# Optimization experiments

Hardware: AMD Instinct MI355X
Metric: run time of the kernel (lower is better)

Reference implementation:

```python
import jax, jax.numpy as jnp
import numpy as np

DIM, EXP = 512, 16
INTERNAL = DIM * EXP  # 8192
BATCH, SEQ = 2, 2048


def setup_inputs() -> dict:
    key = jax.random.key(0)
    ks = jax.random.split(key, 8)
    s = 0.02
    return {
        "x": jax.random.normal(ks[0], (BATCH, SEQ, DIM), jnp.float32),
        "W_dt_w": jax.random.normal(ks[1], (INTERNAL, DIM), jnp.float32) * s,
        "W_dt_b": jnp.zeros((INTERNAL,), jnp.float32),
        "W_B_w": jax.random.normal(ks[2], (INTERNAL, DIM), jnp.float32) * s,
        "W_B_b": jnp.zeros((INTERNAL,), jnp.float32),
        "W_C_w": jax.random.normal(ks[3], (INTERNAL, DIM), jnp.float32) * s,
        "W_C_b": jnp.zeros((INTERNAL,), jnp.float32),
        "W_V_w": jax.random.normal(ks[4], (INTERNAL, DIM), jnp.float32) * s,
        "W_V_b": jnp.zeros((INTERNAL,), jnp.float32),
        # A_log = -rand(internal): negative for stability, as in torch init
        "A_log": -jax.random.uniform(ks[5], (INTERNAL,), jnp.float32),
        "W_out_w": jax.random.normal(ks[6], (DIM, INTERNAL), jnp.float32) * s,
        "W_out_b": jnp.zeros((DIM,), jnp.float32),
    }


def _scan_combine(c1, c2):
    # semi-separable recurrence h_t = a_t * h_{t-1} + b_t, as associative op
    a1, b1 = c1
    a2, b2 = c2
    return a2 * a1, a2 * b1 + b2


def reference(x, W_dt_w, W_dt_b, W_B_w, W_B_b, W_C_w, W_C_b,
              W_V_w, W_V_b, A_log, W_out_w, W_out_b):
    # Featurizer10: discretized SSM features. Shapes: x [b,s,d] -> [b,s,n]
    dt = jax.nn.softplus(jnp.einsum('bsd,nd->bsn', x, W_dt_w) + W_dt_b)
    A_bar = jnp.exp(dt * A_log)                                  # S: [b,s,n]
    B_bar = dt * (jnp.einsum('bsd,nd->bsn', x, W_B_w) + W_B_b)   # B: [b,s,n]
    C = jnp.einsum('bsd,nd->bsn', x, W_C_w) + W_C_b              # C: [b,s,n]
    V = jnp.einsum('bsd,nd->bsn', x, W_V_w) + W_V_b              # V: [b,s,n]
    # Token mixing: h_t = A_bar_t * h_{t-1} + B_bar_t * V_t (parallel scan)
    u = B_bar * V
    _, h = jax.lax.associative_scan(_scan_combine, (A_bar, u), axis=1)
    y = C * h                                                    # [b,s,n]
    # Output projection back to model dim
    return jnp.einsum('bsn,dn->bsd', y, W_out_w) + W_out_b
```

## Files before the change

kernel.cpp:

```cpp
#include <hip/hip_runtime.h>

#define DIMK 512
#define NCH  8192
#define MTOT 4096
#define SEQL 2048
#define KS   4

typedef __attribute__((ext_vector_type(8))) short bf16x8;
typedef __attribute__((ext_vector_type(4))) float f32x4;
typedef unsigned int uint32;

__device__ __forceinline__ unsigned short f2bf(float f) {
  unsigned int u = __float_as_uint(f);
  u += 0x7fffu + ((u >> 16) & 1u);
  return (unsigned short)(u >> 16);
}
__device__ __forceinline__ float bf2f(unsigned short v) {
  return __uint_as_float(((unsigned int)v) << 16);
}

struct CvtArgs {
  const float* src[6];
  unsigned short* dst[6];
  int cum[7];
};
__global__ __launch_bounds__(256) void cvt_all_kernel(CvtArgs a, int tot) {
  const int stride = gridDim.x * 256;
  for (int i = blockIdx.x * 256 + threadIdx.x; i < tot; i += stride) {
    int s = 0;
    while (i >= a.cum[s + 1]) ++s;
    const int j = i - a.cum[s];
    const float4* sp = reinterpret_cast<const float4*>(a.src[s]);
    float4 v0 = sp[2 * j], v1 = sp[2 * j + 1];
    union { unsigned short us[8]; uint4 v; } o;
    o.us[0] = f2bf(v0.x); o.us[1] = f2bf(v0.y); o.us[2] = f2bf(v0.z); o.us[3] = f2bf(v0.w);
    o.us[4] = f2bf(v1.x); o.us[5] = f2bf(v1.y); o.us[6] = f2bf(v1.z); o.us[7] = f2bf(v1.w);
    reinterpret_cast<uint4*>(a.dst[s])[j] = o.v;
  }
}

__device__ __forceinline__ int swz(int row, int q) { return q ^ ((row >> 2) & 3); }

#define PLDS_A 4096
#define PLDS_W 8192
#define PLDS   (PLDS_A + PLDS_W)
__global__ __launch_bounds__(256) void proj_kernel(
    const unsigned short* __restrict__ xb,
    const unsigned short* __restrict__ w4,
    const float* __restrict__ b_dt, const float* __restrict__ b_B,
    const float* __restrict__ b_C, const float* __restrict__ b_V,
    const float* __restrict__ A_log,
    uint32* __restrict__ au,
    unsigned short* __restrict__ c_out)
{
  __shared__ __align__(16) unsigned short lds[2][PLDS];
  const int tid = threadIdx.x;
  const int lane = tid & 63;
  const int wave = tid >> 6;
  const int wr = wave >> 1, wc = wave & 1;
  const int n0 = blockIdx.x * 64;
  const int m0 = blockIdx.y * 128;

  auto stage = [&](int buf, int kt) {
    const int k0 = kt * 32;
    #pragma unroll
    for (int i = 0; i < 2; ++i) {
      int c = i * 256 + tid;
      int row = c >> 2, q = c & 3;
      const unsigned short* g = xb + (size_t)(m0 + row) * DIMK + k0 + swz(row, q) * 8;
      __builtin_amdgcn_global_load_lds(
          (const __attribute__((address_space(1))) void*)g,
          (__attribute__((address_space(3))) void*)&lds[buf][c * 8], 16, 0, 0);
    }
    #pragma unroll
    for (int p = 0; p < 4; ++p) {
      int row = tid >> 2, q = tid & 3;
      const unsigned short* g = w4 + ((size_t)p * NCH + n0 + row) * DIMK + k0 + swz(row, q) * 8;
      __builtin_amdgcn_global_load_lds(
          (const __attribute__((address_space(1))) void*)g,
          (__attribute__((address_space(3))) void*)&lds[buf][PLDS_A + p * 2048 + tid * 8], 16, 0, 0);
    }
  };

  f32x4 acc[4][4][2];
  #pragma unroll
  for (int p = 0; p < 4; ++p)
    #pragma unroll
    for (int fm = 0; fm < 4; ++fm)
      #pragma unroll
      for (int fn = 0; fn < 2; ++fn)
        acc[p][fm][fn] = (f32x4){0.f, 0.f, 0.f, 0.f};

  stage(0, 0);
  constexpr int NKT = DIMK / 32;
  #pragma unroll 1
  for (int kt = 0; kt < NKT; ++kt) {
    const int buf = kt & 1;
    if (kt + 1 < NKT) {
      stage(buf ^ 1, kt + 1);
      asm volatile("s_waitcnt vmcnt(6)" ::: "memory");
    } else {
      asm volatile("s_waitcnt vmcnt(0)" ::: "memory");
    }
    __builtin_amdgcn_s_barrier();

    const int arow = wr * 64 + (lane & 15);
    const int qq = lane >> 4;
    bf16x8 af[4];
    #pragma unroll
    for (int fm = 0; fm < 4; ++fm) {
      const int r = arow + fm * 16;
      af[fm] = *reinterpret_cast<const bf16x8*>(&lds[buf][r * 32 + swz(r, qq) * 8]);
    }
    #pragma unroll
    for (int p = 0; p < 4; ++p) {
      bf16x8 bfr[2];
      #pragma unroll
      for (int fn = 0; fn < 2; ++fn) {
        const int r = wc * 32 + fn * 16 + (lane & 15);
        bfr[fn] = *reinterpret_cast<const bf16x8*>(
            &lds[buf][PLDS_A + p * 2048 + r * 32 + swz(r, qq) * 8]);
      }
      __builtin_amdgcn_s_setprio(1);
      #pragma unroll
      for (int fm = 0; fm < 4; ++fm)
        #pragma unroll
        for (int fn = 0; fn < 2; ++fn)
          acc[p][fm][fn] = __builtin_amdgcn_mfma_f32_16x16x32_bf16(
              af[fm], bfr[fn], acc[p][fm][fn], 0, 0, 0);
      __builtin_amdgcn_s_setprio(0);
    }
    asm volatile("s_waitcnt lgkmcnt(0)" ::: "memory");
    __builtin_amdgcn_s_barrier();
  }

  #pragma unroll
  for (int fn = 0; fn < 2; ++fn) {
    const int n = n0 + wc * 32 + fn * 16 + (lane & 15);
    const float vbdt = b_dt[n], vbB = b_B[n], vbC = b_C[n], vbV = b_V[n];
    const float al = A_log[n];
    #pragma unroll
    for (int fm = 0; fm < 4; ++fm) {
      const int mbase = m0 + wr * 64 + fm * 16 + (lane >> 4) * 4;
      #pragma unroll
      for (int r = 0; r < 4; ++r) {
        const size_t off = (size_t)(mbase + r) * NCH + n;
        const float zdt = acc[0][fm][fn][r] + vbdt;
        const float zB  = acc[1][fm][fn][r] + vbB;
        const float zC  = acc[2][fm][fn][r] + vbC;
        const float zV  = acc[3][fm][fn][r] + vbV;
        const float dt = (zdt > 15.f) ? zdt : __logf(1.f + __expf(zdt));
        au[off] = ((uint32)f2bf(dt * al) << 16) | (uint32)f2bf(dt * zB * zV);
        c_out[off] = f2bf(zC);
      }
    }
  }
}

#define SCH 16
#define CSTEPS 128
__global__ __launch_bounds__(1024) void scan_kernel(
    const uint32* __restrict__ au,
    unsigned short* cy)
{
  __shared__ float Ap[SCH][64], He[SCH][64], H0[SCH][64];
  const int lane = threadIdx.x & 63;
  const int w = threadIdx.x >> 6;
  const int c = blockIdx.x * 64 + lane;
  const size_t base = (size_t)blockIdx.y * SEQL * NCH + (size_t)(w * CSTEPS) * NCH + c;

  {
    const uint32* ap = au + base;
    float h = 0.f, vsum = 0.f;
    #pragma unroll 1
    for (int s = 0; s < CSTEPS; s += 8) {
      uint32 wv[8];
      #pragma unroll
      for (int i = 0; i < 8; ++i) wv[i] = ap[(size_t)(s + i) * NCH];
      #pragma unroll
      for (int i = 0; i < 8; ++i) {
        const float av = bf2f((unsigned short)(wv[i] >> 16));
        const float uv = bf2f((unsigned short)(wv[i] & 0xffff));
        vsum += av;
        h = fmaf(__expf(av), h, uv);
      }
    }
    Ap[w][lane] = __expf(vsum);
    He[w][lane] = h;
  }
  __syncthreads();
  if (w == 0) {
    float run = 0.f;
    #pragma unroll
    for (int jj = 0; jj < SCH; ++jj) {
      H0[jj][lane] = run;
      run = fmaf(Ap[jj][lane], run, He[jj][lane]);
    }
  }
  __syncthreads();
  {
    const uint32* ap = au + base;
    unsigned short* cp = cy + base;
    float h = H0[w][lane];
    #pragma unroll 1
    for (int s = 0; s < CSTEPS; s += 8) {
      uint32 wv[8];
      float cv[8];
      #pragma unroll
      for (int i = 0; i < 8; ++i) {
        wv[i] = ap[(size_t)(s + i) * NCH];
        cv[i] = bf2f(cp[(size_t)(s + i) * NCH]);
      }
      #pragma unroll
      for (int i = 0; i < 8; ++i) {
        const float av = bf2f((unsigned short)(wv[i] >> 16));
        const float uv = bf2f((unsigned short)(wv[i] & 0xffff));
        h = fmaf(__expf(av), h, uv);
        cv[i] *= h;
      }
      #pragma unroll
      for (int i = 0; i < 8; ++i) cp[(size_t)(s + i) * NCH] = f2bf(cv[i]);
    }
  }
}

#define OLDS_A 4096
#define OLDS_B 2048
#define OLDS   (OLDS_A + OLDS_B)
__global__ __launch_bounds__(256) void outproj_kernel(
    const unsigned short* __restrict__ yb,
    const unsigned short* __restrict__ wout,
    float* __restrict__ partial)
{
  __shared__ __align__(16) unsigned short lds[2][OLDS];
  const int tid = threadIdx.x;
  const int lane = tid & 63;
  const int wave = tid >> 6;
  const int wr = wave >> 1, wc = wave & 1;
  const int m0 = blockIdx.x * 128;
  const int d0 = blockIdx.y * 64;
  const int kbase = blockIdx.z * (NCH / KS);

  auto stage = [&](int buf, int kt) {
    const int k0 = kbase + kt * 32;
    #pragma unroll
    for (int i = 0; i < 2; ++i) {
      int c = i * 256 + tid;
      int row = c >> 2, q = c & 3;
      const unsigned short* g = yb + (size_t)(m0 + row) * NCH + k0 + swz(row, q) * 8;
      __builtin_amdgcn_global_load_lds(
          (const __attribute__((address_space(1))) void*)g,
          (__attribute__((address_space(3))) void*)&lds[buf][c * 8], 16, 0, 0);
    }
    {
      int row = tid >> 2, q = tid & 3;
      const unsigned short* g = wout + (size_t)(d0 + row) * NCH + k0 + swz(row, q) * 8;
      __builtin_amdgcn_global_load_lds(
          (const __attribute__((address_space(1))) void*)g,
          (__attribute__((address_space(3))) void*)&lds[buf][OLDS_A + tid * 8], 16, 0, 0);
    }
  };

  f32x4 acc[4][2];
  #pragma unroll
  for (int fm = 0; fm < 4; ++fm)
    #pragma unroll
    for (int fn = 0; fn < 2; ++fn) acc[fm][fn] = (f32x4){0.f, 0.f, 0.f, 0.f};

  stage(0, 0);
  constexpr int NKT = (NCH / KS) / 32;
  #pragma unroll 1
  for (int kt = 0; kt < NKT; ++kt) {
    const int buf = kt & 1;
    if (kt + 1 < NKT) {
      stage(buf ^ 1, kt + 1);
      asm volatile("s_waitcnt vmcnt(3)" ::: "memory");
    } else {
      asm volatile("s_waitcnt vmcnt(0)" ::: "memory");
    }
    __builtin_amdgcn_s_barrier();

    const int qq = lane >> 4;
    bf16x8 af[4], bfr[2];
    #pragma unroll
    for (int fm = 0; fm < 4; ++fm) {
      const int r = wr * 64 + fm * 16 + (lane & 15);
      af[fm] = *reinterpret_cast<const bf16x8*>(&lds[buf][r * 32 + swz(r, qq) * 8]);
    }
    #pragma unroll
    for (int fn = 0; fn < 2; ++fn) {
      const int r = wc * 32 + fn * 16 + (lane & 15);
      bfr[fn] = *reinterpret_cast<const bf16x8*>(
          &lds[buf][OLDS_A + r * 32 + swz(r, qq) * 8]);
    }
    __builtin_amdgcn_s_setprio(1);
    #pragma unroll
    for (int fm = 0; fm < 4; ++fm)
      #pragma unroll
      for (int fn = 0; fn < 2; ++fn)
        acc[fm][fn] = __builtin_amdgcn_mfma_f32_16x16x32_bf16(
            af[fm], bfr[fn], acc[fm][fn], 0, 0, 0);
    __builtin_amdgcn_s_setprio(0);
    asm volatile("s_waitcnt lgkmcnt(0)" ::: "memory");
    __builtin_amdgcn_s_barrier();
  }

  float* pout = partial + (size_t)blockIdx.z * MTOT * DIMK;
  #pragma unroll
  for (int fn = 0; fn < 2; ++fn) {
    const int d = d0 + wc * 32 + fn * 16 + (lane & 15);
    #pragma unroll
    for (int fm = 0; fm < 4; ++fm) {
      const int mbase = m0 + wr * 64 + fm * 16 + (lane >> 4) * 4;
      #pragma unroll
      for (int r = 0; r < 4; ++r)
        pout[(size_t)(mbase + r) * DIMK + d] = acc[fm][fn][r];
    }
  }
}

__global__ __launch_bounds__(256) void reduce_kernel(
    const float* __restrict__ p, const float* __restrict__ bias,
    float* __restrict__ out)
{
  const int i = blockIdx.x * 256 + threadIdx.x;
  const float4* p4 = reinterpret_cast<const float4*>(p);
  float4 s = p4[i];
  #pragma unroll
  for (int k = 1; k < KS; ++k) {
    float4 t = p4[(size_t)k * (MTOT * DIMK / 4) + i];
    s.x += t.x; s.y += t.y; s.z += t.z; s.w += t.w;
  }
  const float4 b = reinterpret_cast<const float4*>(bias)[i & 127];
  s.x += b.x; s.y += b.y; s.z += b.z; s.w += b.w;
  reinterpret_cast<float4*>(out)[i] = s;
}

extern "C" void kernel_launch(void* const* d_in, const int* in_sizes, int n_in,
                              void* d_out, int out_size, void* d_ws, size_t ws_size,
                              hipStream_t stream) {
  const float* x    = (const float*)d_in[0];
  const float* Wdt  = (const float*)d_in[1];
  const float* bdt  = (const float*)d_in[2];
  const float* WB   = (const float*)d_in[3];
  const float* bB   = (const float*)d_in[4];
  const float* WC   = (const float*)d_in[5];
  const float* bC   = (const float*)d_in[6];
  const float* WV   = (const float*)d_in[7];
  const float* bV   = (const float*)d_in[8];
  const float* Alog = (const float*)d_in[9];
  const float* Wout = (const float*)d_in[10];
  const float* bout = (const float*)d_in[11];
  float* out = (float*)d_out;

  char* ws = (char*)d_ws;
  unsigned short* woutb = (unsigned short*)(ws);
  unsigned short* xb    = (unsigned short*)(ws + 8388608);
  unsigned short* w4    = (unsigned short*)(ws + 12582912);
  char* dyn = ws + 46137344;
  uint32*         au  = (uint32*)(dyn);
  unsigned short* cy  = (unsigned short*)(dyn + (size_t)MTOT * NCH * 4);
  float* partial = (float*)au;

  CvtArgs ca;
  ca.src[0] = x;    ca.dst[0] = xb;
  ca.src[1] = Wdt;  ca.dst[1] = w4 + 0 * 4194304;
  ca.src[2] = WB;   ca.dst[2] = w4 + 1 * 4194304;
  ca.src[3] = WC;   ca.dst[3] = w4 + 2 * 4194304;
  ca.src[4] = WV;   ca.dst[4] = w4 + 3 * 4194304;
  ca.src[5] = Wout; ca.dst[5] = woutb;
  ca.cum[0] = 0;        ca.cum[1] = 262144;  ca.cum[2] = 786432;
  ca.cum[3] = 1310720;  ca.cum[4] = 1835008; ca.cum[5] = 2359296;
  ca.cum[6] = 2883584;
  cvt_all_kernel<<<2048, 256, 0, stream>>>(ca, 2883584);

  proj_kernel<<<dim3(NCH / 64, MTOT / 128), 256, 0, stream>>>(
      xb, w4, bdt, bB, bC, bV, Alog, au, cy);
  scan_kernel<<<dim3(NCH / 64, 2), 1024, 0, stream>>>(au, cy);
  outproj_kernel<<<dim3(MTOT / 128, DIMK / 64, KS), 256, 0, stream>>>(
      cy, woutb, partial);
  reduce_kernel<<<MTOT * DIMK / 4 / 256, 256, 0, stream>>>(partial, bout, out);
}
```

Measured before the change: 488.2 us.

## Interleave projection weights and enlarge proj GEMM tile to 256x256 with 8 waves

```diff
diff --git a/kernel.cpp b/kernel.cpp
--- a/kernel.cpp
+++ b/kernel.cpp
@@ -2,6 +2,7 @@
 
 #define DIMK 512
 #define NCH  8192
+#define NCAT 32768
 #define MTOT 4096
 #define SEQL 2048
 #define KS   4
@@ -35,124 +36,131 @@
     union { unsigned short us[8]; uint4 v; } o;
     o.us[0] = f2bf(v0.x); o.us[1] = f2bf(v0.y); o.us[2] = f2bf(v0.z); o.us[3] = f2bf(v0.w);
     o.us[4] = f2bf(v1.x); o.us[5] = f2bf(v1.y); o.us[6] = f2bf(v1.z); o.us[7] = f2bf(v1.w);
-    reinterpret_cast<uint4*>(a.dst[s])[j] = o.v;
-  }
-}
-
-__device__ __forceinline__ int swz(int row, int q) { return q ^ ((row >> 2) & 3); }
-
-#define PLDS_A 4096
-#define PLDS_W 8192
-#define PLDS   (PLDS_A + PLDS_W)
-__global__ __launch_bounds__(256) void proj_kernel(
+    int dj = j;
+    if (s >= 1 && s <= 4) {
+      const int row = j >> 6, k8 = j & 63, p = s - 1;
+      const int ncat = (row >> 4) * 64 + (p << 4) + (row & 15);
+      dj = ncat * 64 + k8;
+    }
+    reinterpret_cast<uint4*>(a.dst[s])[dj] = o.v;
+  }
+}
+
+__global__ __launch_bounds__(512) void proj_kernel(
     const unsigned short* __restrict__ xb,
-    const unsigned short* __restrict__ w4,
+    const unsigned short* __restrict__ wcat,
     const float* __restrict__ b_dt, const float* __restrict__ b_B,
     const float* __restrict__ b_C, const float* __restrict__ b_V,
     const float* __restrict__ A_log,
     uint32* __restrict__ au,
     unsigned short* __restrict__ c_out)
 {
-  __shared__ __align__(16) unsigned short lds[2][PLDS];
+  __shared__ __align__(16) unsigned short lds_all[65536];
+  unsigned short* ldsA = lds_all;
+  unsigned short* ldsB = lds_all + 32768;
+
   const int tid = threadIdx.x;
   const int lane = tid & 63;
   const int wave = tid >> 6;
-  const int wr = wave >> 1, wc = wave & 1;
-  const int n0 = blockIdx.x * 64;
-  const int m0 = blockIdx.y * 128;
-
-  auto stage = [&](int buf, int kt) {
-    const int k0 = kt * 32;
+  const int wr = wave >> 2;
+  const int wc = wave & 3;
+  const int l15 = lane & 15, l4 = lane >> 4;
+  const int bx = blockIdx.x;
+  const int m0 = blockIdx.y * 256;
+
+  auto stage_half = [&](int bsel, int kt, int kind) {
+    const int k0 = kt * 64;
     #pragma unroll
     for (int i = 0; i < 2; ++i) {
-      int c = i * 256 + tid;
-      int row = c >> 2, q = c & 3;
-      const unsigned short* g = xb + (size_t)(m0 + row) * DIMK + k0 + swz(row, q) * 8;
-      __builtin_amdgcn_global_load_lds(
-          (const __attribute__((address_space(1))) void*)g,
-          (__attribute__((address_space(3))) void*)&lds[buf][c * 8], 16, 0, 0);
-    }
-    #pragma unroll
-    for (int p = 0; p < 4; ++p) {
-      int row = tid >> 2, q = tid & 3;
-      const unsigned short* g = w4 + ((size_t)p * NCH + n0 + row) * DIMK + k0 + swz(row, q) * 8;
-      __builtin_amdgcn_global_load_lds(
-          (const __attribute__((address_space(1))) void*)g,
-          (__attribute__((address_space(3))) void*)&lds[buf][PLDS_A + p * 2048 + tid * 8], 16, 0, 0);
+      const int s = i * 512 + tid;
+      const int rl = s >> 3, q = s & 7;
+      const int row = (kind & 1) * 128 + rl;
+      const int ksrc = q ^ (row & 7);
+      if (kind < 2) {
+        const unsigned short* g = xb + (size_t)(m0 + row) * DIMK + k0 + ksrc * 8;
+        __builtin_amdgcn_global_load_lds(
+            (const __attribute__((address_space(1))) void*)g,
+            (__attribute__((address_space(3))) void*)&ldsA[bsel * 16384 + row * 64 + q * 8],
+            16, 0, 0);
+      } else {
+        const unsigned short* g = wcat + (size_t)(bx * 256 + row) * DIMK + k0 + ksrc * 8;
+        __builtin_amdgcn_global_load_lds(
+            (const __attribute__((address_space(1))) void*)g,
+            (__attribute__((address_space(3))) void*)&ldsB[bsel * 16384 + row * 64 + q * 8],
+            16, 0, 0);
+      }
     }
   };
 
-  f32x4 acc[4][4][2];
-  #pragma unroll
-  for (int p = 0; p < 4; ++p)
-    #pragma unroll
-    for (int fm = 0; fm < 4; ++fm)
-      #pragma unroll
-      for (int fn = 0; fn < 2; ++fn)
-        acc[p][fm][fn] = (f32x4){0.f, 0.f, 0.f, 0.f};
-
-  stage(0, 0);
-  constexpr int NKT = DIMK / 32;
+  f32x4 acc[8][4];
+  #pragma unroll
+  for (int fm = 0; fm < 8; ++fm)
+    #pragma unroll
+    for (int fn = 0; fn < 4; ++fn) acc[fm][fn] = (f32x4){0.f, 0.f, 0.f, 0.f};
+
+  stage_half(0, 0, 0); stage_half(0, 0, 1); stage_half(0, 0, 2); stage_half(0, 0, 3);
+
+  constexpr int NT = DIMK / 64;
   #pragma unroll 1
-  for (int kt = 0; kt < NKT; ++kt) {
-    const int buf = kt & 1;
-    if (kt + 1 < NKT) {
-      stage(buf ^ 1, kt + 1);
-      asm volatile("s_waitcnt vmcnt(6)" ::: "memory");
-    } else {
-      asm volatile("s_waitcnt vmcnt(0)" ::: "memory");
-    }
+  for (int t = 0; t < NT; ++t) {
+    const int bsel = t & 1;
+    asm volatile("s_waitcnt vmcnt(0)" ::: "memory");
     __builtin_amdgcn_s_barrier();
-
-    const int arow = wr * 64 + (lane & 15);
-    const int qq = lane >> 4;
-    bf16x8 af[4];
-    #pragma unroll
-    for (int fm = 0; fm < 4; ++fm) {
-      const int r = arow + fm * 16;
-      af[fm] = *reinterpret_cast<const bf16x8*>(&lds[buf][r * 32 + swz(r, qq) * 8]);
-    }
-    #pragma unroll
-    for (int p = 0; p < 4; ++p) {
-      bf16x8 bfr[2];
-      #pragma unroll
-      for (int fn = 0; fn < 2; ++fn) {
-        const int r = wc * 32 + fn * 16 + (lane & 15);
-        bfr[fn] = *reinterpret_cast<const bf16x8*>(
-            &lds[buf][PLDS_A + p * 2048 + r * 32 + swz(r, qq) * 8]);
-      }
+    bf16x8 bfr[4];
+    #pragma unroll
+    for (int ph = 0; ph < 4; ++ph) {
+      const int ks = ph >> 1, fmg = ph & 1;
+      const int qk = ks * 4 + l4;
+      bf16x8 af[4];
+      #pragma unroll
+      for (int i = 0; i < 4; ++i) {
+        const int r = wr * 128 + (fmg * 4 + i) * 16 + l15;
+        af[i] = *reinterpret_cast<const bf16x8*>(
+            &ldsA[bsel * 16384 + r * 64 + (qk ^ (r & 7)) * 8]);
+      }
+      if (fmg == 0) {
+        #pragma unroll
+        for (int fn = 0; fn < 4; ++fn) {
+          const int rb = wc * 64 + fn * 16 + l15;
+          bfr[fn] = *reinterpret_cast<const bf16x8*>(
+              &ldsB[bsel * 16384 + rb * 64 + (qk ^ (rb & 7)) * 8]);
+        }
+      }
+      if (t + 1 < NT && ph < 2) {
+        stage_half(bsel ^ 1, t + 1, ph * 2 + 0);
+        stage_half(bsel ^ 1, t + 1, ph * 2 + 1);
+      }
+      __builtin_amdgcn_s_barrier();
+      asm volatile("s_waitcnt lgkmcnt(0)" ::: "memory");
+      __builtin_amdgcn_sched_barrier(0);
       __builtin_amdgcn_s_setprio(1);
       #pragma unroll
-      for (int fm = 0; fm < 4; ++fm)
+      for (int i = 0; i < 4; ++i)
         #pragma unroll
-        for (int fn = 0; fn < 2; ++fn)
-          acc[p][fm][fn] = __builtin_amdgcn_mfma_f32_16x16x32_bf16(
-              af[fm], bfr[fn], acc[p][fm][fn], 0, 0, 0);
+        for (int fn = 0; fn < 4; ++fn)
+          acc[fmg * 4 + i][fn] = __builtin_amdgcn_mfma_f32_16x16x32_bf16(
+              af[i], bfr[fn], acc[fmg * 4 + i][fn], 0, 0, 0);
       __builtin_amdgcn_s_setprio(0);
-    }
-    asm volatile("s_waitcnt lgkmcnt(0)" ::: "memory");
-    __builtin_amdgcn_s_barrier();
-  }
-
-  #pragma unroll
-  for (int fn = 0; fn < 2; ++fn) {
-    const int n = n0 + wc * 32 + fn * 16 + (lane & 15);
-    const float vbdt = b_dt[n], vbB = b_B[n], vbC = b_C[n], vbV = b_V[n];
-    const float al = A_log[n];
-    #pragma unroll
-    for (int fm = 0; fm < 4; ++fm) {
-      const int mbase = m0 + wr * 64 + fm * 16 + (lane >> 4) * 4;
-      #pragma unroll
-      for (int r = 0; r < 4; ++r) {
-        const size_t off = (size_t)(mbase + r) * NCH + n;
-        const float zdt = acc[0][fm][fn][r] + vbdt;
-        const float zB  = acc[1][fm][fn][r] + vbB;
-        const float zC  = acc[2][fm][fn][r] + vbC;
-        const float zV  = acc[3][fm][fn][r] + vbV;
-        const float dt = (zdt > 15.f) ? zdt : __logf(1.f + __expf(zdt));
-        au[off] = ((uint32)f2bf(dt * al) << 16) | (uint32)f2bf(dt * zB * zV);
-        c_out[off] = f2bf(zC);
-      }
+      __builtin_amdgcn_s_barrier();
+    }
+  }
+
+  const int ch = bx * 64 + wc * 16 + l15;
+  const float vbdt = b_dt[ch], vbB = b_B[ch], vbC = b_C[ch], vbV = b_V[ch];
+  const float al = A_log[ch];
+  #pragma unroll
+  for (int fm = 0; fm < 8; ++fm) {
+    const int mb = m0 + wr * 128 + fm * 16 + l4 * 4;
+    #pragma unroll
+    for (int r = 0; r < 4; ++r) {
+      const size_t off = (size_t)(mb + r) * NCH + ch;
+      const float zdt = acc[fm][0][r] + vbdt;
+      const float zB  = acc[fm][1][r] + vbB;
+      const float zC  = acc[fm][2][r] + vbC;
+      const float zV  = acc[fm][3][r] + vbV;
+      const float dt = (zdt > 15.f) ? zdt : __logf(1.f + __expf(zdt));
+      au[off] = ((uint32)f2bf(dt * al) << 16) | (uint32)f2bf(dt * zB * zV);
+      c_out[off] = f2bf(zC);
     }
   }
 }
@@ -223,6 +231,8 @@
     }
   }
 }
+
+__device__ __forceinline__ int swz(int row, int q) { return q ^ ((row >> 2) & 3); }
 
 #define OLDS_A 4096
 #define OLDS_B 2048
@@ -356,7 +366,7 @@
   char* ws = (char*)d_ws;
   unsigned short* woutb = (unsigned short*)(ws);
   unsigned short* xb    = (unsigned short*)(ws + 8388608);
-  unsigned short* w4    = (unsigned short*)(ws + 12582912);
+  unsigned short* wcat  = (unsigned short*)(ws + 12582912);
   char* dyn = ws + 46137344;
   uint32*         au  = (uint32*)(dyn);
   unsigned short* cy  = (unsigned short*)(dyn + (size_t)MTOT * NCH * 4);
@@ -364,18 +374,18 @@
 
   CvtArgs ca;
   ca.src[0] = x;    ca.dst[0] = xb;
-  ca.src[1] = Wdt;  ca.dst[1] = w4 + 0 * 4194304;
-  ca.src[2] = WB;   ca.dst[2] = w4 + 1 * 4194304;
-  ca.src[3] = WC;   ca.dst[3] = w4 + 2 * 4194304;
-  ca.src[4] = WV;   ca.dst[4] = w4 + 3 * 4194304;
+  ca.src[1] = Wdt;  ca.dst[1] = wcat;
+  ca.src[2] = WB;   ca.dst[2] = wcat;
+  ca.src[3] = WC;   ca.dst[3] = wcat;
+  ca.src[4] = WV;   ca.dst[4] = wcat;
   ca.src[5] = Wout; ca.dst[5] = woutb;
   ca.cum[0] = 0;        ca.cum[1] = 262144;  ca.cum[2] = 786432;
   ca.cum[3] = 1310720;  ca.cum[4] = 1835008; ca.cum[5] = 2359296;
   ca.cum[6] = 2883584;
   cvt_all_kernel<<<2048, 256, 0, stream>>>(ca, 2883584);
 
-  proj_kernel<<<dim3(NCH / 64, MTOT / 128), 256, 0, stream>>>(
-      xb, w4, bdt, bB, bC, bV, Alog, au, cy);
+  proj_kernel<<<dim3(NCAT / 256, MTOT / 256), 512, 0, stream>>>(
+      xb, wcat, bdt, bB, bC, bV, Alog, au, cy);
   scan_kernel<<<dim3(NCH / 64, 2), 1024, 0, stream>>>(au, cy);
   outproj_kernel<<<dim3(MTOT / 128, DIMK / 64, KS), 256, 0, stream>>>(
       cy, woutb, partial);
```

Result: faster. 414.8 us (-15.0%).
